# Optimization experiments

Measured on AMD Instinct MI355X. Metric: run time of the kernel, lower is better.

The kernel has to match this reference:

```python
import jax, jax.numpy as jnp
import numpy as np

B, C, E, H = 8, 2048, 256, 64
N_AGENTS = 4
KAPPA = 0.9
MASKED = True


def _decay_xi_delta(dones):
    """Vectorized equivalent of get_decay_matrix / get_xi / delta.

    dones: [B, C] bool. Timestep dones are dones[:, ::N_AGENTS] -> [B, T].
    The original Python loop builds mask[b,n,m] = exists i with ts_done[b,i]
    and n >= i and m < i, i.e. a done strictly after m and at-or-before n.
    That equals (inclusive_cumsum[n] - inclusive_cumsum[m]) > 0.
    """
    ts = dones[:, ::N_AGENTS]                      # [B, T]
    T = ts.shape[1]
    csum = jnp.cumsum(ts.astype(jnp.int32), axis=1)            # inclusive
    blocked = (csum[:, :, None] - csum[:, None, :]) > 0        # [B, T, T]
    ts_mask = (~blocked).astype(jnp.float32)

    n = jnp.arange(T)
    diff = n[:, None] - n[None, :]
    dm = jnp.where(diff >= 0, KAPPA ** diff.astype(jnp.float32), 0.0)  # [T, T]
    dm = dm[None, :, :] * ts_mask                               # [B, T, T]
    # repeat_interleave over both time axes -> per-agent [B, C, C]
    dm = jnp.repeat(jnp.repeat(dm, N_AGENTS, axis=1), N_AGENTS, axis=2)
    if MASKED:
        Cfull = dm.shape[-1]
        dm = dm * jnp.tril(jnp.ones((Cfull, Cfull), dm.dtype))[None]

    # xi: kappa^(t+1) before the first done, 0 after (per timestep, repeated per agent)
    has_done = jnp.any(ts, axis=1, keepdims=True)               # [B, 1]
    first = jnp.argmax(ts.astype(jnp.float32), axis=1, keepdims=True)
    first = jnp.where(has_done, first, T)                       # [B, 1]
    t_idx = jnp.arange(T)[None, :]                              # [1, T]
    xi = (KAPPA ** (t_idx + 1).astype(jnp.float32)) * (t_idx < first).astype(jnp.float32)
    xi = jnp.repeat(xi, N_AGENTS, axis=1)[:, :, None]           # [B, C, 1]

    delta = (~jnp.any(ts, axis=1)).astype(jnp.float32)[:, None, None]  # [B,1,1]
    return dm, xi, delta


def setup_inputs() -> dict:
    key = jax.random.key(0)
    ks = jax.random.split(key, 8)
    return {
        "key_in": jax.random.normal(ks[0], (B, C, E), jnp.float32),
        "query": jax.random.normal(ks[1], (B, C, E), jnp.float32),
        "value": jax.random.normal(ks[2], (B, C, E), jnp.float32),
        "hstate": jax.random.normal(ks[3], (B, H, H), jnp.float32),
        "dones": jax.random.randint(ks[4], (B, C), 0, 2).astype(bool),
        "w_q": jax.random.normal(ks[5], (E, H), jnp.float32) / np.sqrt(E).astype(np.float32),
        "w_k": jax.random.normal(ks[6], (E, H), jnp.float32) / np.sqrt(E).astype(np.float32),
        "w_v": jax.random.normal(ks[7], (E, H), jnp.float32) / np.sqrt(E).astype(np.float32),
    }


def reference(key_in, query, value, hstate, dones, w_q, w_k, w_v):
    q = query @ w_q                                  # [B, C, H]
    k = key_in @ w_k                                 # [B, C, H]
    v = value @ w_v                                  # [B, C, H]

    dm, xi, delta = _decay_xi_delta(dones)           # [B,C,C], [B,C,1], [B,1,1]
    T = C // N_AGENTS
    chunk_decay = KAPPA ** T

    # next_hstate = k^T @ (v * last_row_of_decay^T) + hstate * chunk_decay * delta
    next_h = jnp.einsum('bch,bcd->bhd', k, v * dm[:, -1, :, None]) \
        + hstate * chunk_decay * delta

    cross = jnp.einsum('bch,bhd->bcd', q, hstate) * xi         # [B, C, H]
    scores = jnp.einsum('bch,bmh->bcm', q, k) * dm              # [B, C, C]
    inner = jnp.einsum('bcm,bmd->bcd', scores, v)               # [B, C, H]
    return inner + cross, next_h
```

## Files before the change

kernel.cpp:

```cpp
#include <hip/hip_runtime.h>
#include <hip/hip_bf16.h>
#include <cstddef>

#define B_ 8
#define C_ 2048
#define E_ 256
#define H_ 64
#define T_ 512
#define NA 4
#define KAPPA 0.9f

typedef __attribute__((ext_vector_type(8))) short bf16x8;
typedef __attribute__((ext_vector_type(4))) float f32x4;

__device__ inline short f2bf(float x) {
    unsigned u = __builtin_bit_cast(unsigned, x);
    u += 0x7fff + ((u >> 16) & 1);
    return (short)(u >> 16);
}

__global__ __launch_bounds__(256) void wt_kernel(
    const float* __restrict__ w_q, const float* __restrict__ w_k,
    const float* __restrict__ w_v, short* __restrict__ wt)
{
    const int mat = blockIdx.x >> 2;
    const int k0  = (blockIdx.x & 3) * 64;
    const float* W = (mat == 0) ? w_q : (mat == 1) ? w_k : w_v;
    __shared__ float tile[64][67];
    const int t = threadIdx.x;
#pragma unroll
    for (int pass = 0; pass < 16; ++pass) {
        int idx = pass * 256 + t;
        int r = idx >> 6, c = idx & 63;
        tile[r][c] = W[(size_t)(k0 + r) * H_ + c];
    }
    __syncthreads();
#pragma unroll
    for (int pass = 0; pass < 16; ++pass) {
        int idx = pass * 256 + t;
        int d = idx >> 6, c = idx & 63;
        wt[(size_t)mat * (H_ * E_) + (size_t)d * E_ + k0 + c] = f2bf(tile[c][d]);
    }
}

__global__ __launch_bounds__(256) void proj_mfma(
    const float* __restrict__ key_in, const float* __restrict__ query,
    const float* __restrict__ value, const short* __restrict__ wt,
    float* __restrict__ qp, float* __restrict__ kp, float* __restrict__ vp)
{
    const int mat = blockIdx.y;
    const float* A; float* O;
    if (mat == 0)      { A = query;  O = qp; }
    else if (mat == 1) { A = key_in; O = kp; }
    else               { A = value;  O = vp; }

    __shared__ short Wt[64][264];

    const int t    = threadIdx.x;
    const int row0 = blockIdx.x * 64;
    const int lane = t & 63;
    const int mt   = t >> 6;
    const int lr   = lane & 15;
    const int lg   = lane >> 4;

    const short* wsrc = wt + (size_t)mat * (H_ * E_);
#pragma unroll
    for (int pass = 0; pass < 8; ++pass) {
        int idx = pass * 2048 + t * 8;
        int d = idx >> 8, k = idx & 255;
        *(bf16x8*)&Wt[d][k] = *(const bf16x8*)&wsrc[idx];
    }
    __syncthreads();

    const float* arow = &A[(size_t)(row0 + mt * 16 + lr) * E_ + lg * 8];

    f32x4 acc[4] = {};
#pragma unroll
    for (int kc = 0; kc < 8; ++kc) {
        f32x4 x0 = *(const f32x4*)(arow + kc * 32);
        f32x4 x1 = *(const f32x4*)(arow + kc * 32 + 4);
        bf16x8 af;
        af[0] = f2bf(x0[0]); af[1] = f2bf(x0[1]);
        af[2] = f2bf(x0[2]); af[3] = f2bf(x0[3]);
        af[4] = f2bf(x1[0]); af[5] = f2bf(x1[1]);
        af[6] = f2bf(x1[2]); af[7] = f2bf(x1[3]);
#pragma unroll
        for (int nt = 0; nt < 4; ++nt) {
            bf16x8 bfrag = *(const bf16x8*)&Wt[nt * 16 + lr][kc * 32 + lg * 8];
            acc[nt] = __builtin_amdgcn_mfma_f32_16x16x32_bf16(af, bfrag, acc[nt], 0, 0, 0);
        }
    }

#pragma unroll
    for (int nt = 0; nt < 4; ++nt)
#pragma unroll
        for (int i = 0; i < 4; ++i)
            O[(size_t)(row0 + mt * 16 + lg * 4 + i) * H_ + nt * 16 + lr] = acc[nt][i];
}

__global__ __launch_bounds__(256) void out_kernel(
    const float* __restrict__ qp, const float* __restrict__ kp,
    const float* __restrict__ vp, const float* __restrict__ hs,
    const unsigned char* __restrict__ raw,
    float* __restrict__ out0, float* __restrict__ outh)
{
    const int t    = threadIdx.x;
    const int lane = t & 63;
    const int idx  = blockIdx.x * 4 + (t >> 6);

    const uint4* dp = (const uint4*)raw;
    uint4 w0 = dp[lane * 2];
    uint4 w1 = dp[lane * 2 + 1];
    unsigned nz = (w0.x | w0.y | w0.z | w0.w | w1.x | w1.y | w1.z | w1.w) & 0xFFFFFF00u;
    const int stride = (__ballot(nz != 0) != 0ULL) ? 1 : 4;

    if (idx < B_ * T_) {
        const int b = idx >> 9;
        const int n = idx & (T_ - 1);
        const int a = lane >> 4;
        const int g = lane & 15;
        const unsigned char* drow = raw + (size_t)b * C_ * stride;

        int s = 0; bool found = false;
        for (int base = n; ; base -= 64) {
            int j = base - lane;
            unsigned long long m =
                __ballot(j >= 0 && drow[(size_t)(4 * j) * stride] != 0);
            if (m) { s = base - __builtin_ctzll(m); found = true; break; }
            if (base < 64) break;
        }

        const float* kb = kp + (size_t)b * C_ * H_;
        const float* vb = vp + (size_t)b * C_ * H_;
        f32x4 q4 = *(const f32x4*)&qp[((size_t)b * C_ + 4 * n + a) * H_ + 4 * g];

        f32x4 acc = {};
#pragma unroll
        for (int ma = 0; ma < NA; ++ma) {
            const int m = 4 * n + ma;
            f32x4 k4 = *(const f32x4*)&kb[(size_t)m * H_ + 4 * g];
            float p = q4[0] * k4[0] + q4[1] * k4[1] + q4[2] * k4[2] + q4[3] * k4[3];
            p += __shfl_xor(p, 1); p += __shfl_xor(p, 2);
            p += __shfl_xor(p, 4); p += __shfl_xor(p, 8);
            if (ma <= a) {
                f32x4 v4 = *(const f32x4*)&vb[(size_t)m * H_ + 4 * g];
                acc[0] += p * v4[0]; acc[1] += p * v4[1];
                acc[2] += p * v4[2]; acc[3] += p * v4[3];
            }
        }
        float decay = KAPPA;
        for (int mt = n - 1; mt >= s; --mt) {
#pragma unroll
            for (int ma = 0; ma < NA; ++ma) {
                const int m = 4 * mt + ma;
                f32x4 k4 = *(const f32x4*)&kb[(size_t)m * H_ + 4 * g];
                float p = q4[0] * k4[0] + q4[1] * k4[1] + q4[2] * k4[2] + q4[3] * k4[3];
                p += __shfl_xor(p, 1); p += __shfl_xor(p, 2);
                p += __shfl_xor(p, 4); p += __shfl_xor(p, 8);
                p *= decay;
                f32x4 v4 = *(const f32x4*)&vb[(size_t)m * H_ + 4 * g];
                acc[0] += p * v4[0]; acc[1] += p * v4[1];
                acc[2] += p * v4[2]; acc[3] += p * v4[3];
            }
            decay *= KAPPA;
        }
        if (!found) {
            const float xi = powf(KAPPA, (float)(n + 1));
            const float* hsb = hs + (size_t)b * H_ * H_;
            f32x4 cacc = {};
#pragma unroll
            for (int h = 0; h < H_; ++h) {
                float qh = __shfl(q4[h & 3], (a << 4) + (h >> 2));
                f32x4 h4 = *(const f32x4*)&hsb[h * H_ + 4 * g];
                cacc[0] += qh * h4[0]; cacc[1] += qh * h4[1];
                cacc[2] += qh * h4[2]; cacc[3] += qh * h4[3];
            }
            acc[0] += xi * cacc[0]; acc[1] += xi * cacc[1];
            acc[2] += xi * cacc[2]; acc[3] += xi * cacc[3];
        }
        *(f32x4*)&out0[((size_t)b * C_ + 4 * n + a) * H_ + 4 * g] = acc;
    } else {
        const int pair = idx - B_ * T_;
        const int b = pair >> 6;
        const int h = pair & (H_ - 1);
        const int d = lane;
        const unsigned char* drow = raw + (size_t)b * C_ * stride;

        int s = 0; bool found = false;
        for (int base = T_ - 1; ; base -= 64) {
            int j = base - lane;
            unsigned long long m =
                __ballot(j >= 0 && drow[(size_t)(4 * j) * stride] != 0);
            if (m) { s = base - __builtin_ctzll(m); found = true; break; }
            if (base < 64) break;
        }

        const float* kb = kp + (size_t)b * C_ * H_;
        const float* vb = vp + (size_t)b * C_ * H_;
        float acc = 0.f, w = 1.f;
        for (int mt = T_ - 1; mt >= s; --mt) {
#pragma unroll
            for (int ma = 0; ma < NA; ++ma) {
                const int m = 4 * mt + ma;
                acc += w * kb[(size_t)m * H_ + h] * vb[(size_t)m * H_ + d];
            }
            w *= KAPPA;
        }
        if (!found)
            acc += hs[((size_t)b * H_ + h) * H_ + d] * powf(KAPPA, (float)T_);
        outh[((size_t)b * H_ + h) * H_ + d] = acc;
    }
}

extern "C" void kernel_launch(void* const* d_in, const int* in_sizes, int n_in,
                              void* d_out, int out_size, void* d_ws, size_t ws_size,
                              hipStream_t stream)
{
    const float* key_in = (const float*)d_in[0];
    const float* query  = (const float*)d_in[1];
    const float* value  = (const float*)d_in[2];
    const float* hstate = (const float*)d_in[3];
    const unsigned char* dones = (const unsigned char*)d_in[4];
    const float* w_q = (const float*)d_in[5];
    const float* w_k = (const float*)d_in[6];
    const float* w_v = (const float*)d_in[7];

    float* qp = (float*)d_ws;
    float* kp = qp + (size_t)B_ * C_ * H_;
    float* vp = kp + (size_t)B_ * C_ * H_;
    short* wt = (short*)(vp + (size_t)B_ * C_ * H_);

    wt_kernel<<<12, 256, 0, stream>>>(w_q, w_k, w_v, wt);
    dim3 pgrid(B_ * C_ / 64, 3);
    proj_mfma<<<pgrid, 256, 0, stream>>>(key_in, query, value, wt, qp, kp, vp);
    out_kernel<<<(B_ * T_ + B_ * H_) / 4, 256, 0, stream>>>(
        qp, kp, vp, hstate, dones,
        (float*)d_out, (float*)d_out + (size_t)B_ * C_ * H_);
}
```

Baseline: 32.68 us.

## Store q projection as bf16, precompute dones stride, replace powf with exp2f

The q projection is now written as bf16 rather than fp32, which halves its write and read traffic. The dones-stride detection moves out of every out_kernel wave into one extra block of the weight-transpose kernel, which writes the result to workspace. powf calls become exp2f or a precomputed constant, and f2bf now uses the library bf16 conversion. The trade-offs are extra rounding on q and a serial scan of 16K bytes in a single block.

```diff
diff --git a/kernel.cpp b/kernel.cpp
--- a/kernel.cpp
+++ b/kernel.cpp
@@ -9,50 +9,67 @@
 #define T_ 512
 #define NA 4
 #define KAPPA 0.9f
+#define LOG2_KAPPA (-0.15200309344504997f)
+#define KAPPA_T 3.73302e-24f
 
 typedef __attribute__((ext_vector_type(8))) short bf16x8;
 typedef __attribute__((ext_vector_type(4))) float f32x4;
 
 __device__ inline short f2bf(float x) {
-    unsigned u = __builtin_bit_cast(unsigned, x);
-    u += 0x7fff + ((u >> 16) & 1);
-    return (short)(u >> 16);
+    return (short)__builtin_bit_cast(unsigned short, __float2bfloat16(x));
+}
+__device__ inline float bf2f(unsigned short u) {
+    return __builtin_bit_cast(float, (unsigned)u << 16);
 }
 
 __global__ __launch_bounds__(256) void wt_kernel(
     const float* __restrict__ w_q, const float* __restrict__ w_k,
-    const float* __restrict__ w_v, short* __restrict__ wt)
-{
-    const int mat = blockIdx.x >> 2;
-    const int k0  = (blockIdx.x & 3) * 64;
-    const float* W = (mat == 0) ? w_q : (mat == 1) ? w_k : w_v;
-    __shared__ float tile[64][67];
+    const float* __restrict__ w_v, short* __restrict__ wt,
+    const unsigned char* __restrict__ raw, int* __restrict__ stridep)
+{
     const int t = threadIdx.x;
-#pragma unroll
-    for (int pass = 0; pass < 16; ++pass) {
-        int idx = pass * 256 + t;
-        int r = idx >> 6, c = idx & 63;
-        tile[r][c] = W[(size_t)(k0 + r) * H_ + c];
-    }
-    __syncthreads();
-#pragma unroll
-    for (int pass = 0; pass < 16; ++pass) {
-        int idx = pass * 256 + t;
-        int d = idx >> 6, c = idx & 63;
-        wt[(size_t)mat * (H_ * E_) + (size_t)d * E_ + k0 + c] = f2bf(tile[c][d]);
+    if (blockIdx.x < 12) {
+        const int mat = blockIdx.x >> 2;
+        const int k0  = (blockIdx.x & 3) * 64;
+        const float* W = (mat == 0) ? w_q : (mat == 1) ? w_k : w_v;
+        __shared__ float tile[64][67];
+#pragma unroll
+        for (int pass = 0; pass < 16; ++pass) {
+            int idx = pass * 256 + t;
+            int r = idx >> 6, c = idx & 63;
+            tile[r][c] = W[(size_t)(k0 + r) * H_ + c];
+        }
+        __syncthreads();
+#pragma unroll
+        for (int pass = 0; pass < 16; ++pass) {
+            int idx = pass * 256 + t;
+            int d = idx >> 6, c = idx & 63;
+            wt[(size_t)mat * (H_ * E_) + (size_t)d * E_ + k0 + c] = f2bf(tile[c][d]);
+        }
+    } else {
+        __shared__ int f;
+        if (t == 0) f = 0;
+        __syncthreads();
+        int local = 0;
+        for (int j = t; j < B_ * C_; j += 256)
+            if ((j & 3) && raw[j]) local = 1;
+        if (local) f = 1;
+        __syncthreads();
+        if (t == 0) *stridep = f ? 1 : 4;
     }
 }
 
 __global__ __launch_bounds__(256) void proj_mfma(
     const float* __restrict__ key_in, const float* __restrict__ query,
     const float* __restrict__ value, const short* __restrict__ wt,
-    float* __restrict__ qp, float* __restrict__ kp, float* __restrict__ vp)
+    unsigned short* __restrict__ qp, float* __restrict__ kp,
+    float* __restrict__ vp)
 {
     const int mat = blockIdx.y;
-    const float* A; float* O;
-    if (mat == 0)      { A = query;  O = qp; }
-    else if (mat == 1) { A = key_in; O = kp; }
-    else               { A = value;  O = vp; }
+    const float* A;
+    if (mat == 0)      A = query;
+    else if (mat == 1) A = key_in;
+    else               A = value;
 
     __shared__ short Wt[64][264];
 
@@ -91,28 +108,33 @@
         }
     }
 
-#pragma unroll
-    for (int nt = 0; nt < 4; ++nt)
-#pragma unroll
-        for (int i = 0; i < 4; ++i)
-            O[(size_t)(row0 + mt * 16 + lg * 4 + i) * H_ + nt * 16 + lr] = acc[nt][i];
+    if (mat == 0) {
+#pragma unroll
+        for (int nt = 0; nt < 4; ++nt)
+#pragma unroll
+            for (int i = 0; i < 4; ++i)
+                qp[(size_t)(row0 + mt * 16 + lg * 4 + i) * H_ + nt * 16 + lr] =
+                    (unsigned short)f2bf(acc[nt][i]);
+    } else {
+        float* O = (mat == 1) ? kp : vp;
+#pragma unroll
+        for (int nt = 0; nt < 4; ++nt)
+#pragma unroll
+            for (int i = 0; i < 4; ++i)
+                O[(size_t)(row0 + mt * 16 + lg * 4 + i) * H_ + nt * 16 + lr] = acc[nt][i];
+    }
 }
 
 __global__ __launch_bounds__(256) void out_kernel(
-    const float* __restrict__ qp, const float* __restrict__ kp,
+    const unsigned short* __restrict__ qp, const float* __restrict__ kp,
     const float* __restrict__ vp, const float* __restrict__ hs,
-    const unsigned char* __restrict__ raw,
+    const unsigned char* __restrict__ raw, const int* __restrict__ stridep,
     float* __restrict__ out0, float* __restrict__ outh)
 {
     const int t    = threadIdx.x;
     const int lane = t & 63;
     const int idx  = blockIdx.x * 4 + (t >> 6);
-
-    const uint4* dp = (const uint4*)raw;
-    uint4 w0 = dp[lane * 2];
-    uint4 w1 = dp[lane * 2 + 1];
-    unsigned nz = (w0.x | w0.y | w0.z | w0.w | w1.x | w1.y | w1.z | w1.w) & 0xFFFFFF00u;
-    const int stride = (__ballot(nz != 0) != 0ULL) ? 1 : 4;
+    const int stride = *stridep;
 
     if (idx < B_ * T_) {
         const int b = idx >> 9;
@@ -132,7 +154,8 @@
 
         const float* kb = kp + (size_t)b * C_ * H_;
         const float* vb = vp + (size_t)b * C_ * H_;
-        f32x4 q4 = *(const f32x4*)&qp[((size_t)b * C_ + 4 * n + a) * H_ + 4 * g];
+        ushort4 qu = *(const ushort4*)&qp[((size_t)b * C_ + 4 * n + a) * H_ + 4 * g];
+        f32x4 q4 = { bf2f(qu.x), bf2f(qu.y), bf2f(qu.z), bf2f(qu.w) };
 
         f32x4 acc = {};
 #pragma unroll
@@ -165,7 +188,7 @@
             decay *= KAPPA;
         }
         if (!found) {
-            const float xi = powf(KAPPA, (float)(n + 1));
+            const float xi = exp2f(LOG2_KAPPA * (float)(n + 1));
             const float* hsb = hs + (size_t)b * H_ * H_;
             f32x4 cacc = {};
 #pragma unroll
@@ -207,7 +230,7 @@
             w *= KAPPA;
         }
         if (!found)
-            acc += hs[((size_t)b * H_ + h) * H_ + d] * powf(KAPPA, (float)T_);
+            acc += hs[((size_t)b * H_ + h) * H_ + d] * KAPPA_T;
         outh[((size_t)b * H_ + h) * H_ + d] = acc;
     }
 }
@@ -225,15 +248,16 @@
     const float* w_k = (const float*)d_in[6];
     const float* w_v = (const float*)d_in[7];
 
-    float* qp = (float*)d_ws;
-    float* kp = qp + (size_t)B_ * C_ * H_;
-    float* vp = kp + (size_t)B_ * C_ * H_;
-    short* wt = (short*)(vp + (size_t)B_ * C_ * H_);
-
-    wt_kernel<<<12, 256, 0, stream>>>(w_q, w_k, w_v, wt);
+    float*          kp = (float*)d_ws;
+    float*          vp = kp + (size_t)B_ * C_ * H_;
+    unsigned short* qp = (unsigned short*)(vp + (size_t)B_ * C_ * H_);
+    short*          wt = (short*)(qp + (size_t)B_ * C_ * H_);
+    int*       stridep = (int*)(wt + 3 * H_ * E_);
+
+    wt_kernel<<<13, 256, 0, stream>>>(w_q, w_k, w_v, wt, dones, stridep);
     dim3 pgrid(B_ * C_ / 64, 3);
     proj_mfma<<<pgrid, 256, 0, stream>>>(key_in, query, value, wt, qp, kp, vp);
     out_kernel<<<(B_ * T_ + B_ * H_) / 4, 256, 0, stream>>>(
-        qp, kp, vp, hstate, dones,
+        qp, kp, vp, hstate, dones, stridep,
         (float*)d_out, (float*)d_out + (size_t)B_ * C_ * H_);
 }
```

Measured after the change: 39.07 us. 19.5% more time.
